# Kernel tuning notes

Measured on AMD Instinct MI355X. Metric: run time of the kernel, lower is better.

Reference implementation:

```python
import jax, jax.numpy as jnp
import numpy as np

TOP_K = 2
TEMP = 1.0  # router_temperature
B, L, D, F, DF, DR, DH, E = 32, 256, 256, 8, 64, 256, 512, 8
DIN = D + DF  # expert/router input: concat(hidden, feat_emb)


def setup_inputs() -> dict:
    key = jax.random.key(0)
    ks = jax.random.split(key, 12)
    gn = lambda k, shape, fan: jax.random.normal(k, shape, dtype=jnp.float32) * (fan ** -0.5)
    return {
        "hidden": jax.random.normal(ks[0], (B, L, D), dtype=jnp.float32),
        "feat": jax.random.uniform(ks[1], (B, L, F), dtype=jnp.float32),
        "W_feat": gn(ks[2], (F, DF), F),
        "b_feat": jnp.zeros((DF,), jnp.float32),
        "Wr1": gn(ks[3], (DIN, DR), DIN),
        "br1": jnp.zeros((DR,), jnp.float32),
        "Wr2": gn(ks[4], (DR, E), DR),
        "br2": jnp.zeros((E,), jnp.float32),
        "We1": gn(ks[5], (E, DIN, DH), DIN),
        "be1": jnp.zeros((E, DH), jnp.float32),
        "We2": gn(ks[6], (E, DH, D), DH),
        "be2": jnp.zeros((E, D), jnp.float32),
    }


def reference(hidden, feat, W_feat, b_feat, Wr1, br1, Wr2, br2, We1, be1, We2, be2):
    # feature embedding
    feat_emb = feat @ W_feat + b_feat                       # [B,L,DF]
    x = jnp.concatenate([hidden, feat_emb], axis=-1)        # [B,L,DIN]

    # token-level learned router with temperature + top-k gating
    hr = jax.nn.gelu(x @ Wr1 + br1)                         # [B,L,DR]
    gate_logits = (hr @ Wr2 + br2) / TEMP                   # [B,L,E]
    topv, topi = jax.lax.top_k(gate_logits, TOP_K)          # [B,L,K]
    w = jax.nn.softmax(topv, axis=-1)                       # renormalized over top-k
    gate_weights = (jax.nn.one_hot(topi, E, dtype=w.dtype) * w[..., None]).sum(-2)  # [B,L,E]

    # experts: per-expert 2-layer MLP (dense compute, sparse combine via gates)
    he = jax.nn.gelu(jnp.einsum('bli,eih->bleh', x, We1) + be1)   # [B,L,E,DH]
    eo = jnp.einsum('bleh,eho->bleo', he, We2) + be2              # [B,L,E,D]
    stage_delta = jnp.einsum('ble,bleo->blo', gate_weights, eo)   # next_hidden - hidden

    return stage_delta, gate_weights, gate_logits
```

## Files before the change

kernel.cpp:

```cpp
#include <hip/hip_runtime.h>
#include <hip/hip_bf16.h>

#define N_TOK   8192
#define DMODEL  256
#define NFEAT   8
#define DFEAT   64
#define DIN     320
#define DRTR    256
#define NE      8
#define DH      512
#define TB      8
#define TE      32

#define OUT_GATEW  (N_TOK*DMODEL)
#define OUT_LOGITS (N_TOK*DMODEL + N_TOK*NE)

typedef short v8s __attribute__((ext_vector_type(8)));
typedef float v4f __attribute__((ext_vector_type(4)));

__device__ __forceinline__ unsigned short f2bf(float f){
  unsigned u = __float_as_uint(f);
  return (unsigned short)((u + 0x7FFFu + ((u>>16)&1u)) >> 16);
}
__device__ __forceinline__ float bf2f(unsigned short h){
  return __uint_as_float(((unsigned)h)<<16);
}

__device__ __forceinline__ float gelu_tanh(float v){
  float u = 0.7978845608028654f * (v + 0.044715f * v * v * v);
  float a = fabsf(u);
  float e = __expf(-2.0f * a);
  float t = (1.0f - e) / (1.0f + e);
  t = copysignf(t, u);
  return 0.5f * v * (1.0f + t);
}

__global__ void k_init(int* __restrict__ cnts){
  if (threadIdx.x < NE) cnts[threadIdx.x] = 0;
}

__global__ __launch_bounds__(256) void k_prep1(const float* __restrict__ W,
                                               unsigned short* __restrict__ dh,
                                               unsigned short* __restrict__ dl){
  int gid = blockIdx.x*256 + threadIdx.x;
  int l = gid & 63; int w = gid >> 6;
  int nt = w & 31; w >>= 5; int kstep = w % 10; int e = w / 10;
  int n = nt*16 + (l&15);
  int kb = kstep*32 + ((l>>4)<<3);
  const float* src = W + ((size_t)e*DIN + kb)*DH + n;
  unsigned short hs[8], ls[8];
  #pragma unroll
  for (int i=0;i<8;i++){
    float v = src[(size_t)i*DH];
    unsigned short h = f2bf(v);
    hs[i] = h; ls[i] = f2bf(v - bf2f(h));
  }
  size_t off = (size_t)gid*8;
  *(v8s*)(dh+off) = *(v8s*)hs;
  *(v8s*)(dl+off) = *(v8s*)ls;
}

__global__ __launch_bounds__(256) void k_prep2(const float* __restrict__ W,
                                               unsigned short* __restrict__ dh,
                                               unsigned short* __restrict__ dl){
  int gid = blockIdx.x*256 + threadIdx.x;
  int l = gid & 63; int w = gid >> 6;
  int nt = w & 15; w >>= 4; int kstep = w & 15; int e = w >> 4;
  int n = nt*16 + (l&15);
  int kb = kstep*32 + ((l>>4)<<3);
  const float* src = W + ((size_t)e*DH + kb)*DMODEL + n;
  unsigned short hs[8], ls[8];
  #pragma unroll
  for (int i=0;i<8;i++){
    float v = src[(size_t)i*DMODEL];
    unsigned short h = f2bf(v);
    hs[i] = h; ls[i] = f2bf(v - bf2f(h));
  }
  size_t off = (size_t)gid*8;
  *(v8s*)(dh+off) = *(v8s*)hs;
  *(v8s*)(dl+off) = *(v8s*)ls;
}

__global__ __launch_bounds__(256) void k_router(
    const float* __restrict__ hidden, const float* __restrict__ feat,
    const float* __restrict__ Wf, const float* __restrict__ bfe,
    const float* __restrict__ Wr1, const float* __restrict__ br1,
    const float* __restrict__ Wr2, const float* __restrict__ br2,
    float* __restrict__ out,
    int* __restrict__ cnts, unsigned* __restrict__ lists, float* __restrict__ topw)
{
  __shared__ float x_lds[TB*DIN];
  __shared__ float hr_lds[TB*260];
  __shared__ float part_lds[256];
  __shared__ float lg_lds[TB*NE];
  const int tid = threadIdx.x;
  const int t0 = blockIdx.x * TB;

  {
    float4 z = make_float4(0.f,0.f,0.f,0.f);
    float4* dst = ((float4*)out) + (size_t)blockIdx.x*512 + tid;
    dst[0] = z; dst[256] = z;
  }
  #pragma unroll
  for (int r=0;r<2;r++){
    int idx = r*256 + tid; int t = idx >> 6, lane = idx & 63;
    ((float4*)(x_lds + t*DIN))[lane] =
        ((const float4*)(hidden + (size_t)(t0+t)*DMODEL))[lane];
  }
  #pragma unroll
  for (int r=0;r<2;r++){
    int idx = r*256 + tid; int t = idx >> 6, j = idx & 63;
    float acc = bfe[j];
    #pragma unroll
    for (int f=0; f<NFEAT; f++) acc += feat[(size_t)(t0+t)*NFEAT + f] * Wf[f*DFEAT + j];
    x_lds[t*DIN + DMODEL + j] = acc;
  }
  __syncthreads();

  const int jq = tid & 63;
  const int tg = tid >> 6;
  {
    float4 b4 = ((const float4*)br1)[jq];
    float4 acc0 = b4, acc1 = b4;
    const float4* W1 = ((const float4*)Wr1) + jq;

    auto fma4 = [&](int i4, const float4 (&w)[4]){
      float4 xa = *(const float4*)&x_lds[(tg*2+0)*DIN + i4*4];
      float4 xb = *(const float4*)&x_lds[(tg*2+1)*DIN + i4*4];
      acc0.x += xa.x*w[0].x + xa.y*w[1].x + xa.z*w[2].x + xa.w*w[3].x;
      acc0.y += xa.x*w[0].y + xa.y*w[1].y + xa.z*w[2].y + xa.w*w[3].y;
      acc0.z += xa.x*w[0].z + xa.y*w[1].z + xa.z*w[2].z + xa.w*w[3].z;
      acc0.w += xa.x*w[0].w + xa.y*w[1].w + xa.z*w[2].w + xa.w*w[3].w;
      acc1.x += xb.x*w[0].x + xb.y*w[1].x + xb.z*w[2].x + xb.w*w[3].x;
      acc1.y += xb.x*w[0].y + xb.y*w[1].y + xb.z*w[2].y + xb.w*w[3].y;
      acc1.z += xb.x*w[0].z + xb.y*w[1].z + xb.z*w[2].z + xb.w*w[3].z;
      acc1.w += xb.x*w[0].w + xb.y*w[1].w + xb.z*w[2].w + xb.w*w[3].w;
    };
    auto ld = [&](float4 (&b)[4], int c){
      #pragma unroll
      for (int r=0;r<4;r++) b[r] = W1[(c*4+r)*64];
    };
    float4 b0[4], b1[4], b2[4], b3[4];
    ld(b0,0); ld(b1,1); ld(b2,2); ld(b3,3);
    for (int c=0; c<80; c+=4){
      fma4(c+0,b0); if (c+4<80) ld(b0,c+4);
      fma4(c+1,b1); if (c+5<80) ld(b1,c+5);
      fma4(c+2,b2); if (c+6<80) ld(b2,c+6);
      fma4(c+3,b3); if (c+7<80) ld(b3,c+7);
    }
    *(float4*)&hr_lds[(tg*2+0)*260 + jq*4] =
        make_float4(gelu_tanh(acc0.x),gelu_tanh(acc0.y),gelu_tanh(acc0.z),gelu_tanh(acc0.w));
    *(float4*)&hr_lds[(tg*2+1)*260 + jq*4] =
        make_float4(gelu_tanh(acc1.x),gelu_tanh(acc1.y),gelu_tanh(acc1.z),gelu_tanh(acc1.w));
  }
  __syncthreads();
  {
    int q = tid >> 6, rr = tid & 63, t = rr >> 3, e = rr & 7;
    float a0=0.f, a1=0.f, a2=0.f, a3=0.f;
    #pragma unroll 4
    for (int k4=0;k4<16;k4++){
      float4 h4 = ((const float4*)hr_lds)[t*65 + q*16 + k4];
      int row = q*64 + k4*4;
      a0 += h4.x * Wr2[(row+0)*NE + e];
      a1 += h4.y * Wr2[(row+1)*NE + e];
      a2 += h4.z * Wr2[(row+2)*NE + e];
      a3 += h4.w * Wr2[(row+3)*NE + e];
    }
    part_lds[tid] = (a0+a1)+(a2+a3);
  }
  __syncthreads();
  if (tid < TB*NE){
    int t = tid >> 3, e = tid & 7;
    float lg = br2[e] + part_lds[tid] + part_lds[tid+64] + part_lds[tid+128] + part_lds[tid+192];
    out[OUT_LOGITS + (size_t)(t0+t)*NE + e] = lg;
    lg_lds[t*NE + e] = lg;
  }
  __syncthreads();
  if (tid < TB){
    int t = tid;
    float v1 = lg_lds[t*NE]; int i1 = 0;
    #pragma unroll
    for (int e=1;e<NE;e++){ float v = lg_lds[t*NE+e]; if (v > v1){ v1 = v; i1 = e; } }
    float v2 = -3.4e38f; int i2 = -1;
    #pragma unroll
    for (int e=0;e<NE;e++){
      if (e == i1) continue;
      float v = lg_lds[t*NE+e]; if (v > v2){ v2 = v; i2 = e; }
    }
    float d   = expf(v2 - v1);
    float inv = 1.0f/(1.0f + d);
    float w1 = inv, w2 = d*inv;
    #pragma unroll
    for (int e=0;e<NE;e++){
      float gv = (e==i1) ? w1 : ((e==i2) ? w2 : 0.f);
      out[OUT_GATEW + (size_t)(t0+t)*NE + e] = gv;
    }
    int p1 = atomicAdd(&cnts[i1], 1);
    lists[i1*N_TOK + p1] = (unsigned)(((t0+t)<<1));
    int p2 = atomicAdd(&cnts[i2], 1);
    lists[i2*N_TOK + p2] = (unsigned)(((t0+t)<<1) | 1);
    topw[(t0+t)*2]   = w1;
    topw[(t0+t)*2+1] = w2;
  }
}

#define XLOFF 10496
#define HELOFF 16640
__global__ __launch_bounds__(256) void k_expert(
    const float* __restrict__ hidden, const float* __restrict__ feat,
    const float* __restrict__ Wf, const float* __restrict__ bfe,
    const int* __restrict__ cnts, const unsigned* __restrict__ lists,
    const float* __restrict__ topw,
    const unsigned short* __restrict__ W1h, const unsigned short* __restrict__ W1l,
    const unsigned short* __restrict__ W2h, const unsigned short* __restrict__ W2l,
    const float* __restrict__ be1, const float* __restrict__ be2,
    float* __restrict__ out)
{
  __shared__ unsigned short sm[33280];
  __shared__ int   tok_lds[TE];
  __shared__ float w_lds[TE];

  const int e    = blockIdx.x & 7;
  const int tile = blockIdx.x >> 3;
  const int cnt  = cnts[e];
  const int start = tile * TE;
  if (start >= cnt) return;
  const int ntk = min(TE, cnt - start);
  const int tid = threadIdx.x;

  if (tid < TE){
    if (tid < ntk){
      unsigned ent = lists[e*N_TOK + start + tid];
      int tok = (int)(ent >> 1);
      tok_lds[tid] = tok;
      w_lds[tid]   = topw[tok*2 + (ent & 1)];
    } else { tok_lds[tid] = -1; w_lds[tid] = 0.f; }
  }
  __syncthreads();
  {
    int lane = tid & 63, tq = tid >> 6;
    #pragma unroll
    for (int r=0;r<8;r++){
      int t = r*4 + tq;
      int tok = tok_lds[t];
      float4 h4 = make_float4(0.f,0.f,0.f,0.f);
      if (tok >= 0) h4 = ((const float4*)(hidden + (size_t)tok*DMODEL))[lane];
      unsigned short h0=f2bf(h4.x),h1=f2bf(h4.y),h2=f2bf(h4.z),h3=f2bf(h4.w);
      unsigned short l0=f2bf(h4.x-bf2f(h0)),l1=f2bf(h4.y-bf2f(h1)),
                     l2=f2bf(h4.z-bf2f(h2)),l3=f2bf(h4.w-bf2f(h3));
      uint2 hp, lp;
      hp.x = (unsigned)h0 | ((unsigned)h1<<16); hp.y = (unsigned)h2 | ((unsigned)h3<<16);
      lp.x = (unsigned)l0 | ((unsigned)l1<<16); lp.y = (unsigned)l2 | ((unsigned)l3<<16);
      *(uint2*)&sm[t*328 + lane*4]         = hp;
      *(uint2*)&sm[XLOFF + t*328 + lane*4] = lp;
    }
  }
  #pragma unroll
  for (int r=0;r<8;r++){
    int idx = r*256 + tid; int t = idx >> 6, j = idx & 63;
    int tok = tok_lds[t];
    float acc = 0.f;
    if (tok >= 0){
      acc = bfe[j];
      #pragma unroll
      for (int f=0; f<NFEAT; f++) acc += feat[(size_t)tok*NFEAT + f] * Wf[f*DFEAT + j];
    }
    unsigned short h = f2bf(acc);
    sm[t*328 + DMODEL + j]         = h;
    sm[XLOFF + t*328 + DMODEL + j] = f2bf(acc - bf2f(h));
  }
  __syncthreads();

  const int wv = tid >> 6;
  const int l  = tid & 63;
  const int lg = l >> 4;
  const int lr = l & 15;

  auto mm6 = [&](v4f &c0, v4f &c1, v8s ah0, v8s ah1, v8s al0, v8s al1, v8s bh, v8s bl){
    c0 = __builtin_amdgcn_mfma_f32_16x16x32_bf16(ah0, bh, c0, 0,0,0);
    c1 = __builtin_amdgcn_mfma_f32_16x16x32_bf16(ah1, bh, c1, 0,0,0);
    c0 = __builtin_amdgcn_mfma_f32_16x16x32_bf16(al0, bh, c0, 0,0,0);
    c1 = __builtin_amdgcn_mfma_f32_16x16x32_bf16(al1, bh, c1, 0,0,0);
    c0 = __builtin_amdgcn_mfma_f32_16x16x32_bf16(ah0, bl, c0, 0,0,0);
    c1 = __builtin_amdgcn_mfma_f32_16x16x32_bf16(ah1, bl, c1, 0,0,0);
  };

  v4f acc1[2][8];
  {
    v4f z = {0.f,0.f,0.f,0.f};
    #pragma unroll
    for (int m=0;m<2;m++)
      #pragma unroll
      for (int j=0;j<8;j++) acc1[m][j] = z;
    const unsigned short* p1h = W1h + (size_t)e*163840;
    const unsigned short* p1l = W1l + (size_t)e*163840;
    auto ldB1 = [&](int ks, int jh, v8s (&bh)[4], v8s (&bl)[4]){
      #pragma unroll
      for (int j=0;j<4;++j){
        size_t boff = ((size_t)(ks*32 + wv*8 + jh*4 + j)*64 + l)*8;
        bh[j] = *(const v8s*)(p1h + boff);
        bl[j] = *(const v8s*)(p1l + boff);
      }
    };
    v8s bh_a[4], bl_a[4], bh_b[4], bl_b[4];
    ldB1(0,0,bh_a,bl_a);
    for (int ks=0; ks<10; ++ks){
      v8s ah0 = *(const v8s*)&sm[( 0+lr)*328 + ks*32 + lg*8];
      v8s ah1 = *(const v8s*)&sm[(16+lr)*328 + ks*32 + lg*8];
      v8s al0 = *(const v8s*)&sm[XLOFF + ( 0+lr)*328 + ks*32 + lg*8];
      v8s al1 = *(const v8s*)&sm[XLOFF + (16+lr)*328 + ks*32 + lg*8];
      ldB1(ks,1,bh_b,bl_b);
      #pragma unroll
      for (int j=0;j<4;++j) mm6(acc1[0][j], acc1[1][j], ah0,ah1,al0,al1, bh_a[j], bl_a[j]);
      if (ks<9) ldB1(ks+1,0,bh_a,bl_a);
      #pragma unroll
      for (int j=0;j<4;++j) mm6(acc1[0][4+j], acc1[1][4+j], ah0,ah1,al0,al1, bh_b[j], bl_b[j]);
    }
  }
  __syncthreads();
  {
    #pragma unroll
    for (int j=0;j<8;++j){
      int col = (wv*8+j)*16 + lr;
      float b1 = be1[e*DH + col];
      #pragma unroll
      for (int m=0;m<2;m++)
        #pragma unroll
        for (int r=0;r<4;r++){
          float v = gelu_tanh(acc1[m][j][r] + b1);
          int row = m*16 + lg*4 + r;
          unsigned short h = f2bf(v);
          sm[row*520 + col]          = h;
          sm[HELOFF + row*520 + col] = f2bf(v - bf2f(h));
        }
    }
  }
  __syncthreads();
  v4f acc2[2][4];
  {
    v4f z = {0.f,0.f,0.f,0.f};
    #pragma unroll
    for (int m=0;m<2;m++)
      #pragma unroll
      for (int j=0;j<4;j++) acc2[m][j] = z;
    const unsigned short* p2h = W2h + (size_t)e*131072;
    const unsigned short* p2l = W2l + (size_t)e*131072;
    auto ldB2 = [&](int ks, v8s (&bh)[4], v8s (&bl)[4]){
      #pragma unroll
      for (int j=0;j<4;++j){
        size_t boff = ((size_t)(ks*16 + wv*4 + j)*64 + l)*8;
        bh[j] = *(const v8s*)(p2h + boff);
        bl[j] = *(const v8s*)(p2l + boff);
      }
    };
    v8s bh_a[4], bl_a[4], bh_b[4], bl_b[4];
    ldB2(0,bh_a,bl_a);
    for (int ks=0; ks<16; ks+=2){
      v8s ah0 = *(const v8s*)&sm[( 0+lr)*520 + ks*32 + lg*8];
      v8s ah1 = *(const v8s*)&sm[(16+lr)*520 + ks*32 + lg*8];
      v8s al0 = *(const v8s*)&sm[HELOFF + ( 0+lr)*520 + ks*32 + lg*8];
      v8s al1 = *(const v8s*)&sm[HELOFF + (16+lr)*520 + ks*32 + lg*8];
      ldB2(ks+1, bh_b, bl_b);
      #pragma unroll
      for (int j=0;j<4;++j) mm6(acc2[0][j], acc2[1][j], ah0,ah1,al0,al1, bh_a[j], bl_a[j]);
      v8s ch0 = *(const v8s*)&sm[( 0+lr)*520 + (ks+1)*32 + lg*8];
      v8s ch1 = *(const v8s*)&sm[(16+lr)*520 + (ks+1)*32 + lg*8];
      v8s cl0 = *(const v8s*)&sm[HELOFF + ( 0+lr)*520 + (ks+1)*32 + lg*8];
      v8s cl1 = *(const v8s*)&sm[HELOFF + (16+lr)*520 + (ks+1)*32 + lg*8];
      if (ks+2<16) ldB2(ks+2, bh_a, bl_a);
      #pragma unroll
      for (int j=0;j<4;++j) mm6(acc2[0][j], acc2[1][j], ch0,ch1,cl0,cl1, bh_b[j], bl_b[j]);
    }
  }
  {
    #pragma unroll
    for (int j=0;j<4;++j){
      int col = (wv*4+j)*16 + lr;
      float b2 = be2[e*DMODEL + col];
      #pragma unroll
      for (int m=0;m<2;m++)
        #pragma unroll
        for (int r=0;r<4;r++){
          int row = m*16 + lg*4 + r;
          if (row < ntk){
            float w = w_lds[row];
            atomicAdd(out + (size_t)tok_lds[row]*DMODEL + col,
                      w*(acc2[m][j][r] + b2));
          }
        }
    }
  }
}

extern "C" void kernel_launch(void* const* d_in, const int* in_sizes, int n_in,
                              void* d_out, int out_size, void* d_ws, size_t ws_size,
                              hipStream_t stream)
{
  (void)in_sizes; (void)n_in; (void)out_size; (void)ws_size;
  const float* hidden = (const float*)d_in[0];
  const float* feat   = (const float*)d_in[1];
  const float* Wf     = (const float*)d_in[2];
  const float* bfe    = (const float*)d_in[3];
  const float* Wr1    = (const float*)d_in[4];
  const float* br1    = (const float*)d_in[5];
  const float* Wr2    = (const float*)d_in[6];
  const float* br2    = (const float*)d_in[7];
  const float* We1    = (const float*)d_in[8];
  const float* be1    = (const float*)d_in[9];
  const float* We2    = (const float*)d_in[10];
  const float* be2    = (const float*)d_in[11];
  float* out = (float*)d_out;

  char* ws = (char*)d_ws;
  int*      cnts  = (int*)ws;
  unsigned* lists = (unsigned*)(ws + 256);
  float*    topw  = (float*)(ws + 262400);
  unsigned short* W1h = (unsigned short*)(ws + 327936);
  unsigned short* W1l = (unsigned short*)(ws + 2949376);
  unsigned short* W2h = (unsigned short*)(ws + 5570816);
  unsigned short* W2l = (unsigned short*)(ws + 7667968);

  hipLaunchKernelGGL(k_init, dim3(1), dim3(64), 0, stream, cnts);
  hipLaunchKernelGGL(k_prep1, dim3(640), dim3(256), 0, stream, We1, W1h, W1l);
  hipLaunchKernelGGL(k_prep2, dim3(512), dim3(256), 0, stream, We2, W2h, W2l);
  hipLaunchKernelGGL(k_router, dim3(N_TOK/TB), dim3(256), 0, stream,
                     hidden, feat, Wf, bfe, Wr1, br1, Wr2, br2,
                     out, cnts, lists, topw);
  hipLaunchKernelGGL(k_expert, dim3((N_TOK/TE)*NE), dim3(256), 0, stream,
                     hidden, feat, Wf, bfe, cnts, lists, topw,
                     W1h, W1l, W2h, W2l, be1, be2, out);
}
```

Measured before the change: 313.4 us.

## Move router first layer to split-bf16 MFMA with exact fp32 fix-up for near-ties

Replaces the scalar fp32 router GEMM with a bf16 hi/lo split MFMA kernel over 32-token blocks, with the router weights pre-split by a new prep kernel. Tokens whose second and third logits fall within a small threshold are deferred to a fp32 recompute kernel and a gate fix-up kernel, so top-k selection stays consistent with the reference. The expert kernel also moves to 512 threads with fewer accumulators per wave. This aims to cut router compute time, at the cost of extra launches, a capped fix-up list, and possible logit precision differences.

```diff
diff --git a/kernel.cpp b/kernel.cpp
--- a/kernel.cpp
+++ b/kernel.cpp
@@ -9,8 +9,10 @@
 #define DRTR    256
 #define NE      8
 #define DH      512
-#define TB      8
 #define TE      32
+#define RTB     32
+#define FIXCAP  128
+#define FIXTHR  2e-3f
 
 #define OUT_GATEW  (N_TOK*DMODEL)
 #define OUT_LOGITS (N_TOK*DMODEL + N_TOK*NE)
@@ -25,7 +27,6 @@
 __device__ __forceinline__ float bf2f(unsigned short h){
   return __uint_as_float(((unsigned)h)<<16);
 }
-
 __device__ __forceinline__ float gelu_tanh(float v){
   float u = 0.7978845608028654f * (v + 0.044715f * v * v * v);
   float a = fabsf(u);
@@ -35,8 +36,9 @@
   return 0.5f * v * (1.0f + t);
 }
 
-__global__ void k_init(int* __restrict__ cnts){
+__global__ void k_init(int* __restrict__ cnts, int* __restrict__ nfix){
   if (threadIdx.x < NE) cnts[threadIdx.x] = 0;
+  if (threadIdx.x == NE) *nfix = 0;
 }
 
 __global__ __launch_bounds__(256) void k_prep1(const float* __restrict__ W,
@@ -81,132 +83,260 @@
   *(v8s*)(dl+off) = *(v8s*)ls;
 }
 
-__global__ __launch_bounds__(256) void k_router(
+__global__ __launch_bounds__(256) void k_prepr(const float* __restrict__ W,
+                                               unsigned short* __restrict__ dh,
+                                               unsigned short* __restrict__ dl){
+  int gid = blockIdx.x*256 + threadIdx.x;
+  if (gid >= 10240) return;
+  int l = gid & 63; int w = gid >> 6;
+  int nt = w & 15; int kstep = w >> 4;
+  int n = nt*16 + (l&15);
+  int kb = kstep*32 + ((l>>4)<<3);
+  const float* src = W + (size_t)kb*DRTR + n;
+  unsigned short hs[8], ls[8];
+  #pragma unroll
+  for (int i=0;i<8;i++){
+    float v = src[(size_t)i*DRTR];
+    unsigned short h = f2bf(v);
+    hs[i] = h; ls[i] = f2bf(v - bf2f(h));
+  }
+  size_t off = (size_t)gid*8;
+  *(v8s*)(dh+off) = *(v8s*)hs;
+  *(v8s*)(dl+off) = *(v8s*)ls;
+}
+
+#define MM6(c0,c1,ah0,ah1,al0,al1,bh,bl) do{ \
+  c0 = __builtin_amdgcn_mfma_f32_16x16x32_bf16(ah0, bh, c0, 0,0,0); \
+  c1 = __builtin_amdgcn_mfma_f32_16x16x32_bf16(ah1, bh, c1, 0,0,0); \
+  c0 = __builtin_amdgcn_mfma_f32_16x16x32_bf16(al0, bh, c0, 0,0,0); \
+  c1 = __builtin_amdgcn_mfma_f32_16x16x32_bf16(al1, bh, c1, 0,0,0); \
+  c0 = __builtin_amdgcn_mfma_f32_16x16x32_bf16(ah0, bl, c0, 0,0,0); \
+  c1 = __builtin_amdgcn_mfma_f32_16x16x32_bf16(ah1, bl, c1, 0,0,0); }while(0)
+
+#define XLOFF  10496
+#define HELOFF 16640
+
+__global__ __launch_bounds__(512) void k_rmfma(
+    const float* __restrict__ hidden, const float* __restrict__ feat,
+    const float* __restrict__ Wf, const float* __restrict__ bfe,
+    const unsigned short* __restrict__ Wr1h, const unsigned short* __restrict__ Wr1l,
+    const float* __restrict__ br1,
+    const float* __restrict__ Wr2, const float* __restrict__ br2,
+    float* __restrict__ out,
+    int* __restrict__ cnts, unsigned* __restrict__ lists, float* __restrict__ topw,
+    int* __restrict__ nfix, int* __restrict__ fixlist)
+{
+  __shared__ unsigned short sm[21248];
+  __shared__ float part_lds[512];
+  __shared__ float lg_lds[RTB*NE];
+  float* hrf = (float*)sm;
+  const int tid = threadIdx.x;
+  const int t0 = blockIdx.x * RTB;
+
+  {
+    float4 z = make_float4(0.f,0.f,0.f,0.f);
+    float4* dst = ((float4*)out) + (size_t)blockIdx.x*2048 + tid;
+    #pragma unroll
+    for (int r=0;r<4;r++) dst[r*512] = z;
+  }
+  #pragma unroll
+  for (int r=0;r<4;r++){
+    int idx = r*512 + tid; int t = idx >> 6, lane = idx & 63;
+    float4 h4 = ((const float4*)(hidden + (size_t)(t0+t)*DMODEL))[lane];
+    unsigned short h0=f2bf(h4.x),h1=f2bf(h4.y),h2=f2bf(h4.z),h3=f2bf(h4.w);
+    unsigned short l0=f2bf(h4.x-bf2f(h0)),l1=f2bf(h4.y-bf2f(h1)),
+                   l2=f2bf(h4.z-bf2f(h2)),l3=f2bf(h4.w-bf2f(h3));
+    uint2 hp, lp;
+    hp.x=(unsigned)h0|((unsigned)h1<<16); hp.y=(unsigned)h2|((unsigned)h3<<16);
+    lp.x=(unsigned)l0|((unsigned)l1<<16); lp.y=(unsigned)l2|((unsigned)l3<<16);
+    *(uint2*)&sm[t*328 + lane*4]         = hp;
+    *(uint2*)&sm[XLOFF + t*328 + lane*4] = lp;
+  }
+  #pragma unroll
+  for (int r=0;r<4;r++){
+    int idx = r*512 + tid; int t = idx >> 6, j = idx & 63;
+    float acc = bfe[j];
+    #pragma unroll
+    for (int f=0; f<NFEAT; f++) acc += feat[(size_t)(t0+t)*NFEAT + f] * Wf[f*DFEAT + j];
+    unsigned short h = f2bf(acc);
+    sm[t*328 + DMODEL + j]         = h;
+    sm[XLOFF + t*328 + DMODEL + j] = f2bf(acc - bf2f(h));
+  }
+  __syncthreads();
+
+  const int wv = tid >> 6;
+  const int l  = tid & 63;
+  const int lg = l >> 4;
+  const int lr = l & 15;
+
+  v4f acc[2][2];
+  {
+    v4f z = {0.f,0.f,0.f,0.f};
+    acc[0][0]=z; acc[0][1]=z; acc[1][0]=z; acc[1][1]=z;
+    v8s bh_a[2], bl_a[2], bh_b[2], bl_b[2];
+    auto ldBr = [&](int ks, v8s (&bh)[2], v8s (&bl)[2]){
+      #pragma unroll
+      for (int j=0;j<2;++j){
+        size_t boff = ((size_t)(ks*16 + wv*2 + j)*64 + l)*8;
+        bh[j] = *(const v8s*)(Wr1h + boff);
+        bl[j] = *(const v8s*)(Wr1l + boff);
+      }
+    };
+    ldBr(0, bh_a, bl_a);
+    for (int ks=0; ks<10; ks+=2){
+      v8s ah0 = *(const v8s*)&sm[( 0+lr)*328 + ks*32 + lg*8];
+      v8s ah1 = *(const v8s*)&sm[(16+lr)*328 + ks*32 + lg*8];
+      v8s al0 = *(const v8s*)&sm[XLOFF + ( 0+lr)*328 + ks*32 + lg*8];
+      v8s al1 = *(const v8s*)&sm[XLOFF + (16+lr)*328 + ks*32 + lg*8];
+      ldBr(ks+1, bh_b, bl_b);
+      #pragma unroll
+      for (int j=0;j<2;++j) MM6(acc[0][j],acc[1][j], ah0,ah1,al0,al1, bh_a[j],bl_a[j]);
+      v8s ch0 = *(const v8s*)&sm[( 0+lr)*328 + (ks+1)*32 + lg*8];
+      v8s ch1 = *(const v8s*)&sm[(16+lr)*328 + (ks+1)*32 + lg*8];
+      v8s cl0 = *(const v8s*)&sm[XLOFF + ( 0+lr)*328 + (ks+1)*32 + lg*8];
+      v8s cl1 = *(const v8s*)&sm[XLOFF + (16+lr)*328 + (ks+1)*32 + lg*8];
+      if (ks+2<10) ldBr(ks+2, bh_a, bl_a);
+      #pragma unroll
+      for (int j=0;j<2;++j) MM6(acc[0][j],acc[1][j], ch0,ch1,cl0,cl1, bh_b[j],bl_b[j]);
+    }
+  }
+  __syncthreads();
+  #pragma unroll
+  for (int j=0;j<2;++j){
+    int col = (wv*2+j)*16 + lr;
+    float b1 = br1[col];
+    #pragma unroll
+    for (int m=0;m<2;m++)
+      #pragma unroll
+      for (int r=0;r<4;r++){
+        int row = m*16 + lg*4 + r;
+        hrf[row*264 + col] = gelu_tanh(acc[m][j][r] + b1);
+      }
+  }
+  __syncthreads();
+  {
+    int q = tid >> 8, rr = tid & 255, t = rr >> 3, e = rr & 7;
+    float a0=0.f,a1=0.f,a2=0.f,a3=0.f;
+    #pragma unroll 4
+    for (int k4=0;k4<32;k4++){
+      float4 h4 = ((const float4*)hrf)[t*66 + q*32 + k4];
+      int row = q*128 + k4*4;
+      a0 += h4.x * Wr2[(row+0)*NE + e];
+      a1 += h4.y * Wr2[(row+1)*NE + e];
+      a2 += h4.z * Wr2[(row+2)*NE + e];
+      a3 += h4.w * Wr2[(row+3)*NE + e];
+    }
+    part_lds[tid] = (a0+a1)+(a2+a3);
+  }
+  __syncthreads();
+  if (tid < RTB*NE){
+    int t = tid >> 3, e = tid & 7;
+    float lgv = br2[e] + part_lds[tid] + part_lds[tid+256];
+    out[OUT_LOGITS + (size_t)(t0+t)*NE + e] = lgv;
+    lg_lds[t*NE + e] = lgv;
+  }
+  __syncthreads();
+  if (tid < RTB){
+    int t = tid, tok = t0 + t;
+    float v1=-3.4e38f, v2=-3.4e38f, v3=-3.4e38f; int i1=-1, i2=-1;
+    #pragma unroll
+    for (int e=0;e<NE;e++){
+      float v = lg_lds[t*NE+e];
+      if (v > v1){ v3=v2; v2=v1; i2=i1; v1=v; i1=e; }
+      else if (v > v2){ v3=v2; v2=v; i2=e; }
+      else if (v > v3){ v3=v; }
+    }
+    bool defer = false;
+    if (v2 - v3 < FIXTHR){
+      int fi = atomicAdd(nfix, 1);
+      if (fi < FIXCAP){ fixlist[fi] = tok; defer = true; }
+    }
+    if (!defer){
+      float d   = expf(v2 - v1);
+      float inv = 1.0f/(1.0f + d);
+      float w1 = inv, w2 = d*inv;
+      #pragma unroll
+      for (int e=0;e<NE;e++){
+        float gv = (e==i1) ? w1 : ((e==i2) ? w2 : 0.f);
+        out[OUT_GATEW + (size_t)tok*NE + e] = gv;
+      }
+      int p1 = atomicAdd(&cnts[i1], 1);
+      lists[i1*N_TOK + p1] = (unsigned)(tok<<1);
+      int p2 = atomicAdd(&cnts[i2], 1);
+      lists[i2*N_TOK + p2] = (unsigned)((tok<<1) | 1);
+      topw[tok*2]   = w1;
+      topw[tok*2+1] = w2;
+    }
+  }
+}
+
+__global__ __launch_bounds__(256) void k_fix(
     const float* __restrict__ hidden, const float* __restrict__ feat,
     const float* __restrict__ Wf, const float* __restrict__ bfe,
     const float* __restrict__ Wr1, const float* __restrict__ br1,
     const float* __restrict__ Wr2, const float* __restrict__ br2,
-    float* __restrict__ out,
-    int* __restrict__ cnts, unsigned* __restrict__ lists, float* __restrict__ topw)
+    float* __restrict__ out, const int* __restrict__ nfix, const int* __restrict__ fixlist)
 {
-  __shared__ float x_lds[TB*DIN];
-  __shared__ float hr_lds[TB*260];
-  __shared__ float part_lds[256];
-  __shared__ float lg_lds[TB*NE];
+  int nf = *nfix; if (nf > FIXCAP) nf = FIXCAP;
+  if ((int)blockIdx.x >= nf) return;
+  const int tok = fixlist[blockIdx.x];
   const int tid = threadIdx.x;
-  const int t0 = blockIdx.x * TB;
-
+  __shared__ float xf[DIN];
+  __shared__ float hr[DRTR];
+  if (tid < DMODEL) xf[tid] = hidden[(size_t)tok*DMODEL + tid];
+  if (tid < DFEAT){
+    float acc = bfe[tid];
+    #pragma unroll
+    for (int f=0; f<NFEAT; f++) acc += feat[(size_t)tok*NFEAT + f] * Wf[f*DFEAT + tid];
+    xf[DMODEL + tid] = acc;
+  }
+  __syncthreads();
   {
-    float4 z = make_float4(0.f,0.f,0.f,0.f);
-    float4* dst = ((float4*)out) + (size_t)blockIdx.x*512 + tid;
-    dst[0] = z; dst[256] = z;
-  }
-  #pragma unroll
-  for (int r=0;r<2;r++){
-    int idx = r*256 + tid; int t = idx >> 6, lane = idx & 63;
-    ((float4*)(x_lds + t*DIN))[lane] =
-        ((const float4*)(hidden + (size_t)(t0+t)*DMODEL))[lane];
-  }
-  #pragma unroll
-  for (int r=0;r<2;r++){
-    int idx = r*256 + tid; int t = idx >> 6, j = idx & 63;
-    float acc = bfe[j];
-    #pragma unroll
-    for (int f=0; f<NFEAT; f++) acc += feat[(size_t)(t0+t)*NFEAT + f] * Wf[f*DFEAT + j];
-    x_lds[t*DIN + DMODEL + j] = acc;
-  }
-  __syncthreads();
-
-  const int jq = tid & 63;
-  const int tg = tid >> 6;
-  {
-    float4 b4 = ((const float4*)br1)[jq];
-    float4 acc0 = b4, acc1 = b4;
-    const float4* W1 = ((const float4*)Wr1) + jq;
-
-    auto fma4 = [&](int i4, const float4 (&w)[4]){
-      float4 xa = *(const float4*)&x_lds[(tg*2+0)*DIN + i4*4];
-      float4 xb = *(const float4*)&x_lds[(tg*2+1)*DIN + i4*4];
-      acc0.x += xa.x*w[0].x + xa.y*w[1].x + xa.z*w[2].x + xa.w*w[3].x;
-      acc0.y += xa.x*w[0].y + xa.y*w[1].y + xa.z*w[2].y + xa.w*w[3].y;
-      acc0.z += xa.x*w[0].z + xa.y*w[1].z + xa.z*w[2].z + xa.w*w[3].z;
-      acc0.w += xa.x*w[0].w + xa.y*w[1].w + xa.z*w[2].w + xa.w*w[3].w;
-      acc1.x += xb.x*w[0].x + xb.y*w[1].x + xb.z*w[2].x + xb.w*w[3].x;
-      acc1.y += xb.x*w[0].y + xb.y*w[1].y + xb.z*w[2].y + xb.w*w[3].y;
-      acc1.z += xb.x*w[0].z + xb.y*w[1].z + xb.z*w[2].z + xb.w*w[3].z;
-      acc1.w += xb.x*w[0].w + xb.y*w[1].w + xb.z*w[2].w + xb.w*w[3].w;
-    };
-    auto ld = [&](float4 (&b)[4], int c){
-      #pragma unroll
-      for (int r=0;r<4;r++) b[r] = W1[(c*4+r)*64];
-    };
-    float4 b0[4], b1[4], b2[4], b3[4];
-    ld(b0,0); ld(b1,1); ld(b2,2); ld(b3,3);
-    for (int c=0; c<80; c+=4){
-      fma4(c+0,b0); if (c+4<80) ld(b0,c+4);
-      fma4(c+1,b1); if (c+5<80) ld(b1,c+5);
-      fma4(c+2,b2); if (c+6<80) ld(b2,c+6);
-      fma4(c+3,b3); if (c+7<80) ld(b3,c+7);
-    }
-    *(float4*)&hr_lds[(tg*2+0)*260 + jq*4] =
-        make_float4(gelu_tanh(acc0.x),gelu_tanh(acc0.y),gelu_tanh(acc0.z),gelu_tanh(acc0.w));
-    *(float4*)&hr_lds[(tg*2+1)*260 + jq*4] =
-        make_float4(gelu_tanh(acc1.x),gelu_tanh(acc1.y),gelu_tanh(acc1.z),gelu_tanh(acc1.w));
-  }
-  __syncthreads();
-  {
-    int q = tid >> 6, rr = tid & 63, t = rr >> 3, e = rr & 7;
-    float a0=0.f, a1=0.f, a2=0.f, a3=0.f;
-    #pragma unroll 4
-    for (int k4=0;k4<16;k4++){
-      float4 h4 = ((const float4*)hr_lds)[t*65 + q*16 + k4];
-      int row = q*64 + k4*4;
-      a0 += h4.x * Wr2[(row+0)*NE + e];
-      a1 += h4.y * Wr2[(row+1)*NE + e];
-      a2 += h4.z * Wr2[(row+2)*NE + e];
-      a3 += h4.w * Wr2[(row+3)*NE + e];
-    }
-    part_lds[tid] = (a0+a1)+(a2+a3);
-  }
-  __syncthreads();
-  if (tid < TB*NE){
-    int t = tid >> 3, e = tid & 7;
-    float lg = br2[e] + part_lds[tid] + part_lds[tid+64] + part_lds[tid+128] + part_lds[tid+192];
-    out[OUT_LOGITS + (size_t)(t0+t)*NE + e] = lg;
-    lg_lds[t*NE + e] = lg;
-  }
-  __syncthreads();
-  if (tid < TB){
-    int t = tid;
-    float v1 = lg_lds[t*NE]; int i1 = 0;
-    #pragma unroll
-    for (int e=1;e<NE;e++){ float v = lg_lds[t*NE+e]; if (v > v1){ v1 = v; i1 = e; } }
-    float v2 = -3.4e38f; int i2 = -1;
-    #pragma unroll
-    for (int e=0;e<NE;e++){
-      if (e == i1) continue;
-      float v = lg_lds[t*NE+e]; if (v > v2){ v2 = v; i2 = e; }
-    }
-    float d   = expf(v2 - v1);
-    float inv = 1.0f/(1.0f + d);
-    float w1 = inv, w2 = d*inv;
-    #pragma unroll
-    for (int e=0;e<NE;e++){
-      float gv = (e==i1) ? w1 : ((e==i2) ? w2 : 0.f);
-      out[OUT_GATEW + (size_t)(t0+t)*NE + e] = gv;
-    }
-    int p1 = atomicAdd(&cnts[i1], 1);
-    lists[i1*N_TOK + p1] = (unsigned)(((t0+t)<<1));
-    int p2 = atomicAdd(&cnts[i2], 1);
-    lists[i2*N_TOK + p2] = (unsigned)(((t0+t)<<1) | 1);
-    topw[(t0+t)*2]   = w1;
-    topw[(t0+t)*2+1] = w2;
-  }
-}
-
-#define XLOFF 10496
-#define HELOFF 16640
-__global__ __launch_bounds__(256) void k_expert(
+    float acc = br1[tid];
+    for (int i=0;i<DIN;i++) acc += xf[i] * Wr1[(size_t)i*DRTR + tid];
+    hr[tid] = gelu_tanh(acc);
+  }
+  __syncthreads();
+  if (tid < NE){
+    float acc = br2[tid];
+    for (int i=0;i<DRTR;i++) acc += hr[i] * Wr2[i*NE + tid];
+    out[OUT_LOGITS + (size_t)tok*NE + tid] = acc;
+  }
+}
+
+__global__ void k_gatefix(float* __restrict__ out,
+                          int* __restrict__ cnts, unsigned* __restrict__ lists,
+                          float* __restrict__ topw,
+                          const int* __restrict__ nfix, const int* __restrict__ fixlist)
+{
+  int nf = *nfix; if (nf > FIXCAP) nf = FIXCAP;
+  int i = threadIdx.x;
+  if (i >= nf) return;
+  int tok = fixlist[i];
+  float v1=-3.4e38f, v2=-3.4e38f; int i1=-1, i2=-1;
+  #pragma unroll
+  for (int e=0;e<NE;e++){
+    float v = out[OUT_LOGITS + (size_t)tok*NE + e];
+    if (v > v1){ v2=v1; i2=i1; v1=v; i1=e; }
+    else if (v > v2){ v2=v; i2=e; }
+  }
+  float d   = expf(v2 - v1);
+  float inv = 1.0f/(1.0f + d);
+  float w1 = inv, w2 = d*inv;
+  #pragma unroll
+  for (int e=0;e<NE;e++){
+    float gv = (e==i1) ? w1 : ((e==i2) ? w2 : 0.f);
+    out[OUT_GATEW + (size_t)tok*NE + e] = gv;
+  }
+  int p1 = atomicAdd(&cnts[i1], 1);
+  lists[i1*N_TOK + p1] = (unsigned)(tok<<1);
+  int p2 = atomicAdd(&cnts[i2], 1);
+  lists[i2*N_TOK + p2] = (unsigned)((tok<<1) | 1);
+  topw[tok*2]   = w1;
+  topw[tok*2+1] = w2;
+}
+
+__global__ __launch_bounds__(512) void k_expert(
     const float* __restrict__ hidden, const float* __restrict__ feat,
     const float* __restrict__ Wf, const float* __restrict__ bfe,
     const int* __restrict__ cnts, const unsigned* __restrict__ lists,
@@ -237,27 +367,24 @@
     } else { tok_lds[tid] = -1; w_lds[tid] = 0.f; }
   }
   __syncthreads();
-  {
-    int lane = tid & 63, tq = tid >> 6;
-    #pragma unroll
-    for (int r=0;r<8;r++){
-      int t = r*4 + tq;
-      int tok = tok_lds[t];
-      float4 h4 = make_float4(0.f,0.f,0.f,0.f);
-      if (tok >= 0) h4 = ((const float4*)(hidden + (size_t)tok*DMODEL))[lane];
-      unsigned short h0=f2bf(h4.x),h1=f2bf(h4.y),h2=f2bf(h4.z),h3=f2bf(h4.w);
-      unsigned short l0=f2bf(h4.x-bf2f(h0)),l1=f2bf(h4.y-bf2f(h1)),
-                     l2=f2bf(h4.z-bf2f(h2)),l3=f2bf(h4.w-bf2f(h3));
-      uint2 hp, lp;
-      hp.x = (unsigned)h0 | ((unsigned)h1<<16); hp.y = (unsigned)h2 | ((unsigned)h3<<16);
-      lp.x = (unsigned)l0 | ((unsigned)l1<<16); lp.y = (unsigned)l2 | ((unsigned)l3<<16);
-      *(uint2*)&sm[t*328 + lane*4]         = hp;
-      *(uint2*)&sm[XLOFF + t*328 + lane*4] = lp;
-    }
-  }
-  #pragma unroll
-  for (int r=0;r<8;r++){
-    int idx = r*256 + tid; int t = idx >> 6, j = idx & 63;
+  #pragma unroll
+  for (int r=0;r<4;r++){
+    int idx = r*512 + tid; int t = idx >> 6, lane = idx & 63;
+    int tok = tok_lds[t];
+    float4 h4 = make_float4(0.f,0.f,0.f,0.f);
+    if (tok >= 0) h4 = ((const float4*)(hidden + (size_t)tok*DMODEL))[lane];
+    unsigned short h0=f2bf(h4.x),h1=f2bf(h4.y),h2=f2bf(h4.z),h3=f2bf(h4.w);
+    unsigned short l0=f2bf(h4.x-bf2f(h0)),l1=f2bf(h4.y-bf2f(h1)),
+                   l2=f2bf(h4.z-bf2f(h2)),l3=f2bf(h4.w-bf2f(h3));
+    uint2 hp, lp;
+    hp.x=(unsigned)h0|((unsigned)h1<<16); hp.y=(unsigned)h2|((unsigned)h3<<16);
+    lp.x=(unsigned)l0|((unsigned)l1<<16); lp.y=(unsigned)l2|((unsigned)l3<<16);
+    *(uint2*)&sm[t*328 + lane*4]         = hp;
+    *(uint2*)&sm[XLOFF + t*328 + lane*4] = lp;
+  }
+  #pragma unroll
+  for (int r=0;r<4;r++){
+    int idx = r*512 + tid; int t = idx >> 6, j = idx & 63;
     int tok = tok_lds[t];
     float acc = 0.f;
     if (tok >= 0){
@@ -276,33 +403,24 @@
   const int lg = l >> 4;
   const int lr = l & 15;
 
-  auto mm6 = [&](v4f &c0, v4f &c1, v8s ah0, v8s ah1, v8s al0, v8s al1, v8s bh, v8s bl){
-    c0 = __builtin_amdgcn_mfma_f32_16x16x32_bf16(ah0, bh, c0, 0,0,0);
-    c1 = __builtin_amdgcn_mfma_f32_16x16x32_bf16(ah1, bh, c1, 0,0,0);
-    c0 = __builtin_amdgcn_mfma_f32_16x16x32_bf16(al0, bh, c0, 0,0,0);
-    c1 = __builtin_amdgcn_mfma_f32_16x16x32_bf16(al1, bh, c1, 0,0,0);
-    c0 = __builtin_amdgcn_mfma_f32_16x16x32_bf16(ah0, bl, c0, 0,0,0);
-    c1 = __builtin_amdgcn_mfma_f32_16x16x32_bf16(ah1, bl, c1, 0,0,0);
-  };
-
-  v4f acc1[2][8];
+  v4f acc1[2][4];
   {
     v4f z = {0.f,0.f,0.f,0.f};
     #pragma unroll
     for (int m=0;m<2;m++)
       #pragma unroll
-      for (int j=0;j<8;j++) acc1[m][j] = z;
+      for (int j=0;j<4;j++) acc1[m][j] = z;
     const unsigned short* p1h = W1h + (size_t)e*163840;
     const unsigned short* p1l = W1l + (size_t)e*163840;
-    auto ldB1 = [&](int ks, int jh, v8s (&bh)[4], v8s (&bl)[4]){
-      #pragma unroll
-      for (int j=0;j<4;++j){
-        size_t boff = ((size_t)(ks*32 + wv*8 + jh*4 + j)*64 + l)*8;
+    auto ldB1 = [&](int ks, int jh, v8s (&bh)[2], v8s (&bl)[2]){
+      #pragma unroll
+      for (int j=0;j<2;++j){
+        size_t boff = ((size_t)(ks*32 + wv*4 + jh*2 + j)*64 + l)*8;
         bh[j] = *(const v8s*)(p1h + boff);
         bl[j] = *(const v8s*)(p1l + boff);
       }
     };
-    v8s bh_a[4], bl_a[4], bh_b[4], bl_b[4];
+    v8s bh_a[2], bl_a[2], bh_b[2], bl_b[2];
     ldB1(0,0,bh_a,bl_a);
     for (int ks=0; ks<10; ++ks){
       v8s ah0 = *(const v8s*)&sm[( 0+lr)*328 + ks*32 + lg*8];
@@ -311,49 +429,44 @@
       v8s al1 = *(const v8s*)&sm[XLOFF + (16+lr)*328 + ks*32 + lg*8];
       ldB1(ks,1,bh_b,bl_b);
       #pragma unroll
-      for (int j=0;j<4;++j) mm6(acc1[0][j], acc1[1][j], ah0,ah1,al0,al1, bh_a[j], bl_a[j]);
+      for (int j=0;j<2;++j) MM6(acc1[0][j],acc1[1][j], ah0,ah1,al0,al1, bh_a[j],bl_a[j]);
       if (ks<9) ldB1(ks+1,0,bh_a,bl_a);
       #pragma unroll
-      for (int j=0;j<4;++j) mm6(acc1[0][4+j], acc1[1][4+j], ah0,ah1,al0,al1, bh_b[j], bl_b[j]);
-    }
-  }
-  __syncthreads();
-  {
-    #pragma unroll
-    for (int j=0;j<8;++j){
-      int col = (wv*8+j)*16 + lr;
-      float b1 = be1[e*DH + col];
-      #pragma unroll
-      for (int m=0;m<2;m++)
-        #pragma unroll
-        for (int r=0;r<4;r++){
-          float v = gelu_tanh(acc1[m][j][r] + b1);
-          int row = m*16 + lg*4 + r;
-          unsigned short h = f2bf(v);
-          sm[row*520 + col]          = h;
-          sm[HELOFF + row*520 + col] = f2bf(v - bf2f(h));
-        }
-    }
-  }
-  __syncthreads();
-  v4f acc2[2][4];
+      for (int j=0;j<2;++j) MM6(acc1[0][2+j],acc1[1][2+j], ah0,ah1,al0,al1, bh_b[j],bl_b[j]);
+    }
+  }
+  __syncthreads();
+  #pragma unroll
+  for (int j=0;j<4;++j){
+    int col = (wv*4+j)*16 + lr;
+    float b1 = be1[e*DH + col];
+    #pragma unroll
+    for (int m=0;m<2;m++)
+      #pragma unroll
+      for (int r=0;r<4;r++){
+        float v = gelu_tanh(acc1[m][j][r] + b1);
+        int row = m*16 + lg*4 + r;
+        unsigned short h = f2bf(v);
+        sm[row*520 + col]          = h;
+        sm[HELOFF + row*520 + col] = f2bf(v - bf2f(h));
+      }
+  }
+  __syncthreads();
+  v4f acc2[2][2];
   {
     v4f z = {0.f,0.f,0.f,0.f};
-    #pragma unroll
-    for (int m=0;m<2;m++)
-      #pragma unroll
-      for (int j=0;j<4;j++) acc2[m][j] = z;
+    acc2[0][0]=z; acc2[0][1]=z; acc2[1][0]=z; acc2[1][1]=z;
     const unsigned short* p2h = W2h + (size_t)e*131072;
     const unsigned short* p2l = W2l + (size_t)e*131072;
-    auto ldB2 = [&](int ks, v8s (&bh)[4], v8s (&bl)[4]){
-      #pragma unroll
-      for (int j=0;j<4;++j){
-        size_t boff = ((size_t)(ks*16 + wv*4 + j)*64 + l)*8;
+    auto ldB2 = [&](int ks, v8s (&bh)[2], v8s (&bl)[2]){
+      #pragma unroll
+      for (int j=0;j<2;++j){
+        size_t boff = ((size_t)(ks*16 + wv*2 + j)*64 + l)*8;
         bh[j] = *(const v8s*)(p2h + boff);
         bl[j] = *(const v8s*)(p2l + boff);
       }
     };
-    v8s bh_a[4], bl_a[4], bh_b[4], bl_b[4];
+    v8s bh_a[2], bl_a[2], bh_b[2], bl_b[2];
     ldB2(0,bh_a,bl_a);
     for (int ks=0; ks<16; ks+=2){
       v8s ah0 = *(const v8s*)&sm[( 0+lr)*520 + ks*32 + lg*8];
@@ -362,33 +475,31 @@
       v8s al1 = *(const v8s*)&sm[HELOFF + (16+lr)*520 + ks*32 + lg*8];
       ldB2(ks+1, bh_b, bl_b);
       #pragma unroll
-      for (int j=0;j<4;++j) mm6(acc2[0][j], acc2[1][j], ah0,ah1,al0,al1, bh_a[j], bl_a[j]);
+      for (int j=0;j<2;++j) MM6(acc2[0][j],acc2[1][j], ah0,ah1,al0,al1, bh_a[j],bl_a[j]);
       v8s ch0 = *(const v8s*)&sm[( 0+lr)*520 + (ks+1)*32 + lg*8];
       v8s ch1 = *(const v8s*)&sm[(16+lr)*520 + (ks+1)*32 + lg*8];
       v8s cl0 = *(const v8s*)&sm[HELOFF + ( 0+lr)*520 + (ks+1)*32 + lg*8];
       v8s cl1 = *(const v8s*)&sm[HELOFF + (16+lr)*520 + (ks+1)*32 + lg*8];
       if (ks+2<16) ldB2(ks+2, bh_a, bl_a);
       #pragma unroll
-      for (int j=0;j<4;++j) mm6(acc2[0][j], acc2[1][j], ch0,ch1,cl0,cl1, bh_b[j], bl_b[j]);
-    }
-  }
-  {
-    #pragma unroll
-    for (int j=0;j<4;++j){
-      int col = (wv*4+j)*16 + lr;
-      float b2 = be2[e*DMODEL + col];
-      #pragma unroll
-      for (int m=0;m<2;m++)
-        #pragma unroll
-        for (int r=0;r<4;r++){
-          int row = m*16 + lg*4 + r;
-          if (row < ntk){
-            float w = w_lds[row];
-            atomicAdd(out + (size_t)tok_lds[row]*DMODEL + col,
-                      w*(acc2[m][j][r] + b2));
-          }
+      for (int j=0;j<2;++j) MM6(acc2[0][j],acc2[1][j], ch0,ch1,cl0,cl1, bh_b[j],bl_b[j]);
+    }
+  }
+  #pragma unroll
+  for (int j=0;j<2;++j){
+    int col = (wv*2+j)*16 + lr;
+    float b2 = be2[e*DMODEL + col];
+    #pragma unroll
+    for (int m=0;m<2;m++)
+      #pragma unroll
+      for (int r=0;r<4;r++){
+        int row = m*16 + lg*4 + r;
+        if (row < ntk){
+          float w = w_lds[row];
+          atomicAdd(out + (size_t)tok_lds[row]*DMODEL + col,
+                    w*(acc2[m][j][r] + b2));
         }
-    }
+      }
   }
 }
 
@@ -412,21 +523,30 @@
   float* out = (float*)d_out;
 
   char* ws = (char*)d_ws;
-  int*      cnts  = (int*)ws;
-  unsigned* lists = (unsigned*)(ws + 256);
-  float*    topw  = (float*)(ws + 262400);
-  unsigned short* W1h = (unsigned short*)(ws + 327936);
-  unsigned short* W1l = (unsigned short*)(ws + 2949376);
-  unsigned short* W2h = (unsigned short*)(ws + 5570816);
-  unsigned short* W2l = (unsigned short*)(ws + 7667968);
-
-  hipLaunchKernelGGL(k_init, dim3(1), dim3(64), 0, stream, cnts);
+  int*      cnts    = (int*)ws;
+  int*      nfix    = (int*)(ws + 64);
+  int*      fixlist = (int*)(ws + 128);
+  unsigned* lists   = (unsigned*)(ws + 1024);
+  float*    topw    = (float*)(ws + 263168);
+  unsigned short* W1h  = (unsigned short*)(ws + 328704);
+  unsigned short* W1l  = (unsigned short*)(ws + 2950144);
+  unsigned short* W2h  = (unsigned short*)(ws + 5571584);
+  unsigned short* W2l  = (unsigned short*)(ws + 7668736);
+  unsigned short* Wr1h = (unsigned short*)(ws + 9765888);
+  unsigned short* Wr1l = (unsigned short*)(ws + 9929728);
+
+  hipLaunchKernelGGL(k_init, dim3(1), dim3(64), 0, stream, cnts, nfix);
   hipLaunchKernelGGL(k_prep1, dim3(640), dim3(256), 0, stream, We1, W1h, W1l);
   hipLaunchKernelGGL(k_prep2, dim3(512), dim3(256), 0, stream, We2, W2h, W2l);
-  hipLaunchKernelGGL(k_router, dim3(N_TOK/TB), dim3(256), 0, stream,
-                     hidden, feat, Wf, bfe, Wr1, br1, Wr2, br2,
-                     out, cnts, lists, topw);
-  hipLaunchKernelGGL(k_expert, dim3((N_TOK/TE)*NE), dim3(256), 0, stream,
+  hipLaunchKernelGGL(k_prepr, dim3(40),  dim3(256), 0, stream, Wr1, Wr1h, Wr1l);
+  hipLaunchKernelGGL(k_rmfma, dim3(N_TOK/RTB), dim3(512), 0, stream,
+                     hidden, feat, Wf, bfe, Wr1h, Wr1l, br1, Wr2, br2,
+                     out, cnts, lists, topw, nfix, fixlist);
+  hipLaunchKernelGGL(k_fix, dim3(FIXCAP), dim3(256), 0, stream,
+                     hidden, feat, Wf, bfe, Wr1, br1, Wr2, br2, out, nfix, fixlist);
+  hipLaunchKernelGGL(k_gatefix, dim3(1), dim3(FIXCAP), 0, stream,
+                     out, cnts, lists, topw, nfix, fixlist);
+  hipLaunchKernelGGL(k_expert, dim3((N_TOK/TE)*NE), dim3(512), 0, stream,
                      hidden, feat, Wf, bfe, cnts, lists, topw,
                      W1h, W1l, W2h, W2l, be1, be2, out);
 }
```

Result: faster. 293.8 us (-6.2%).
